# Kernel optimization log

Measured on AMD Instinct MI355X. Metric: run time of the kernel, lower is better.

Reference implementation:

```python
import jax, jax.numpy as jnp
import numpy as np


def setup_inputs() -> dict:
    key = jax.random.key(0)
    k1, k2, k3, k4, k5 = jax.random.split(key, 5)
    B, S, IN, OUT, R = 4, 2048, 4096, 4096, 16
    x = jax.random.normal(k1, (B, S, IN), dtype=jnp.float32)
    weight = jax.random.normal(k2, (OUT, IN), dtype=jnp.float32) * 0.02
    bias = jax.random.normal(k3, (OUT,), dtype=jnp.float32) * 0.02
    lora_A = jax.random.normal(k4, (R, IN), dtype=jnp.float32) * 0.02
    lora_B = jax.random.normal(k5, (OUT, R), dtype=jnp.float32) * 0.02
    return {"x": x, "weight": weight, "bias": bias, "lora_A": lora_A, "lora_B": lora_B}


def reference(x, weight, bias, lora_A, lora_B):
    # HiRA (Linear path): out = x @ (W * (1 + A^T B^T)^T)^T + bias
    # prod_AB[i, o] = sum_r A[r, i] * B[o, r]; adapted_weight[o, i] = W[o, i] * (prod_AB + 1)[i, o]
    prod_AB = jnp.einsum('ri,or->io', lora_A, lora_B) + 1.0       # [in, out]
    adapted_weight = weight * prod_AB.T                            # [out, in]
    # F.linear: x @ adapted_weight^T + bias
    return jnp.einsum('bsi,oi->bso', x, adapted_weight) + bias
```

## Files before the change

kernel.cpp:

```cpp
#include <hip/hip_runtime.h>
#include <hip/hip_bf16.h>
#include <stdint.h>

#define M_DIM 8192
#define N_DIM 4096
#define K_DIM 4096
#define R_DIM 16

typedef __bf16 bf16x8 __attribute__((ext_vector_type(8)));
typedef float f32x4 __attribute__((ext_vector_type(4)));
typedef unsigned short u16x8 __attribute__((ext_vector_type(8)));

#define AS1(p) ((const __attribute__((address_space(1))) void*)(p))
#define AS3(p) ((__attribute__((address_space(3))) void*)(p))

#define BAR() do { asm volatile("" ::: "memory"); __builtin_amdgcn_s_barrier(); asm volatile("" ::: "memory"); } while (0)
#define LGKM0() asm volatile("s_waitcnt lgkmcnt(0)" ::: "memory")
#define VMCNT6() asm volatile("s_waitcnt vmcnt(6)" ::: "memory")
#define VMCNT0() asm volatile("s_waitcnt vmcnt(0)" ::: "memory")

__device__ __forceinline__ unsigned short f2bf(float f) {
  unsigned u = __builtin_bit_cast(unsigned, f);
  u += 0x7FFFu + ((u >> 16) & 1u);
  return (unsigned short)(u >> 16);
}

#define CVT_BLOCKS 4096
__global__ void __launch_bounds__(256) prep_kernel(
    const float* __restrict__ x, const float* __restrict__ W,
    const float* __restrict__ lA, const float* __restrict__ lB,
    unsigned short* __restrict__ xb, unsigned short* __restrict__ awb) {
  __shared__ float Asub[16 * 512];
  __shared__ float Bsub[32 * 16];
  const int tid = threadIdx.x;

  if (blockIdx.x < 1024) {
    const int i0 = (blockIdx.x & 7) * 512;
    const int o0 = (blockIdx.x >> 3) * 32;
    for (int idx = tid; idx < 16 * 512; idx += 256) {
      int r = idx >> 9, i = idx & 511;
      Asub[idx] = lA[r * K_DIM + i0 + i];
    }
    for (int idx = tid; idx < 32 * 16; idx += 256) {
      int o = idx >> 4, r = idx & 15;
      Bsub[idx] = lB[(o0 + o) * R_DIM + r];
    }
    __syncthreads();
    for (int idx = tid; idx < 32 * 512; idx += 256) {
      int o = idx >> 9, i = idx & 511;
      float s = 1.0f;
#pragma unroll
      for (int r = 0; r < 16; ++r) s += Asub[r * 512 + i] * Bsub[o * 16 + r];
      size_t g = (size_t)(o0 + o) * K_DIM + i0 + i;
      awb[g] = f2bf(W[g] * s);
    }
  } else {
    const long total = (long)M_DIM * K_DIM;
    long i = ((long)(blockIdx.x - 1024) * 256 + tid) * 8;
    const long stride = (long)CVT_BLOCKS * 256 * 8;
    for (; i < total; i += stride) {
      const float4* p = (const float4*)(x + i);
      float4 f0 = p[0], f1 = p[1];
      u16x8 v;
      v[0] = f2bf(f0.x); v[1] = f2bf(f0.y); v[2] = f2bf(f0.z); v[3] = f2bf(f0.w);
      v[4] = f2bf(f1.x); v[5] = f2bf(f1.y); v[6] = f2bf(f1.z); v[7] = f2bf(f1.w);
      *(u16x8*)(xb + i) = v;
    }
  }
}

__global__ void __launch_bounds__(512, 2) gemm_kernel(
    const unsigned short* __restrict__ Ag,
    const unsigned short* __restrict__ Bg,
    const float* __restrict__ bias,
    float* __restrict__ out) {
  __shared__ __attribute__((aligned(16))) unsigned short LDS[2 * 32768];

  const int nwg = gridDim.x;
  const int q8 = nwg >> 3;
  const int wg = blockIdx.x;
  const int swz = (wg & 7) * q8 + (wg >> 3);
  const int tiles_n = N_DIM / 256;
  const int brow = (swz / tiles_n) * 256;
  const int bcol = (swz % tiles_n) * 256;

  const int tid = threadIdx.x;
  const int lane = tid & 63;
  const int w = tid >> 6;
  const int wr = w >> 2, wc = w & 3;
  const int fr = lane & 15;
  const int kq = (lane >> 4) << 3;

  const int rr = lane >> 2;
  const int cc = ((lane & 1) << 3) | ((((lane >> 1) ^ (lane >> 5)) & 1) << 4);
  const int c_sw = ((w & 1) << 5) | cc;
  const int rbase = ((w >> 1) << 4) + rr;

  const unsigned short* srcA[2][2];
#pragma unroll
  for (int h = 0; h < 2; ++h)
#pragma unroll
    for (int q = 0; q < 2; ++q)
      srcA[h][q] = Ag + (size_t)(brow + h * 128 + q * 64 + rbase) * K_DIM + c_sw;
  const long long bdelta = (long long)(Bg - Ag) + (long long)(bcol - brow) * K_DIM;

  auto stageA = [&](int buf, int h, int kt) {
#pragma unroll
    for (int q = 0; q < 2; ++q)
      __builtin_amdgcn_global_load_lds(AS1(srcA[h][q] + (size_t)kt * 64),
          AS3(&LDS[buf * 32768 + h * 8192 + q * 4096 + w * 512]), 16, 0, 0);
  };
  auto stageB = [&](int buf, int h, int kt) {
#pragma unroll
    for (int q = 0; q < 2; ++q)
      __builtin_amdgcn_global_load_lds(AS1(srcA[h][q] + bdelta + (size_t)kt * 64),
          AS3(&LDS[buf * 32768 + 16384 + h * 8192 + q * 4096 + w * 512]), 16, 0, 0);
  };

  const int rdsw = ((fr << 6) | (kq << 1)) ^ ((fr & 8) << 2);
  auto lda = [&](int buf, int m, int kk) -> bf16x8 {
    return *(const bf16x8*)((const char*)LDS +
        (buf * 65536 + wr * 16384 + (m * 2 + kk) * 1024 + rdsw));
  };
  auto ldb = [&](int buf, int n, int kk) -> bf16x8 {
    return *(const bf16x8*)((const char*)LDS +
        (buf * 65536 + 32768 + (wc >> 1) * 16384 +
         (((wc & 1) * 4 + n) * 2 + kk) * 1024 + rdsw));
  };

  f32x4 acc[8][4] = {};
  bf16x8 a[2][4], b[2][4];

  auto load_a_group = [&](int buf, int mg) {
#pragma unroll
    for (int kk = 0; kk < 2; ++kk)
#pragma unroll
      for (int mi = 0; mi < 4; ++mi)
        a[kk][mi] = lda(buf, mg + mi, kk);
  };
  auto load_b_pair = [&](int buf, int nb) {
#pragma unroll
    for (int kk = 0; kk < 2; ++kk)
#pragma unroll
      for (int ni = 0; ni < 2; ++ni)
        b[kk][nb + ni] = ldb(buf, nb + ni, kk);
  };
  auto mma_quad = [&](int mb, int nb) {
#pragma unroll
    for (int mi = 0; mi < 4; ++mi)
#pragma unroll
      for (int ni = 0; ni < 2; ++ni)
#pragma unroll
        for (int kk = 0; kk < 2; ++kk)
          acc[mb + mi][nb + ni] = __builtin_amdgcn_mfma_f32_16x16x32_bf16(
              a[kk][mi], b[kk][nb + ni], acc[mb + mi][nb + ni], 0, 0, 0);
  };

  stageB(0, 0, 0); stageB(0, 1, 0); stageA(0, 0, 0); stageA(0, 1, 0);
  stageB(1, 0, 1); stageB(1, 1, 1); stageA(1, 0, 1);
  VMCNT6();
  BAR();

#pragma unroll 1
  for (int i = 0; i < K_DIM / 128; ++i) {
    const bool more = (i < K_DIM / 128 - 1);
    const int t_cur1 = 2 * i + 1, t_nx0 = 2 * i + 2, t_nx1 = 2 * i + 3;

    load_a_group(0, 0); load_b_pair(0, 0);
    stageA(1, 1, t_cur1);
    BAR(); LGKM0();
    __builtin_amdgcn_s_setprio(1); mma_quad(0, 0); __builtin_amdgcn_s_setprio(0);
    BAR();
    load_b_pair(0, 2);
    BAR(); LGKM0();
    __builtin_amdgcn_s_setprio(1); mma_quad(0, 2); __builtin_amdgcn_s_setprio(0);
    BAR();
    load_a_group(0, 4);
    if (more) { stageB(0, 0, t_nx0); stageB(0, 1, t_nx0); }
    BAR(); LGKM0();
    __builtin_amdgcn_s_setprio(1); mma_quad(4, 2); __builtin_amdgcn_s_setprio(0);
    BAR();
    if (more) stageA(0, 0, t_nx0);
    BAR();
    __builtin_amdgcn_s_setprio(1); mma_quad(4, 0); __builtin_amdgcn_s_setprio(0);
    if (more) { VMCNT6(); } else { VMCNT0(); }
    BAR();

    load_a_group(1, 0); load_b_pair(1, 0);
    if (more) stageA(0, 1, t_nx0);
    BAR(); LGKM0();
    __builtin_amdgcn_s_setprio(1); mma_quad(0, 0); __builtin_amdgcn_s_setprio(0);
    BAR();
    load_b_pair(1, 2);
    BAR(); LGKM0();
    __builtin_amdgcn_s_setprio(1); mma_quad(0, 2); __builtin_amdgcn_s_setprio(0);
    BAR();
    load_a_group(1, 4);
    if (more) { stageB(1, 0, t_nx1); stageB(1, 1, t_nx1); }
    BAR(); LGKM0();
    __builtin_amdgcn_s_setprio(1); mma_quad(4, 2); __builtin_amdgcn_s_setprio(0);
    BAR();
    if (more) stageA(1, 0, t_nx1);
    BAR();
    __builtin_amdgcn_s_setprio(1); mma_quad(4, 0); __builtin_amdgcn_s_setprio(0);
    if (more) VMCNT6();
    BAR();
  }

  const int fq = (lane >> 4) * 4;
#pragma unroll
  for (int n = 0; n < 4; ++n) {
    const int col = bcol + wc * 64 + n * 16 + fr;
    const float bb = bias[col];
#pragma unroll
    for (int m = 0; m < 8; ++m) {
      const int row = brow + wr * 128 + m * 16 + fq;
      f32x4 v = acc[m][n];
#pragma unroll
      for (int j = 0; j < 4; ++j)
        out[(size_t)(row + j) * N_DIM + col] = v[j] + bb;
    }
  }
}

extern "C" void kernel_launch(void* const* d_in, const int* in_sizes, int n_in,
                              void* d_out, int out_size, void* d_ws, size_t ws_size,
                              hipStream_t stream) {
  const float* x    = (const float*)d_in[0];
  const float* W    = (const float*)d_in[1];
  const float* bias = (const float*)d_in[2];
  const float* lA   = (const float*)d_in[3];
  const float* lB   = (const float*)d_in[4];
  float* out = (float*)d_out;

  unsigned short* xb  = (unsigned short*)d_ws;
  unsigned short* awb = xb + (size_t)M_DIM * K_DIM;

  prep_kernel<<<1024 + CVT_BLOCKS, 256, 0, stream>>>(x, W, lA, lB, xb, awb);
  gemm_kernel<<<(M_DIM / 256) * (N_DIM / 256), 512, 0, stream>>>(xb, awb, bias, out);
}
```

Baseline: 302.6 us.

## Restructure GEMM main loop to prefetch next tile's LDS fragments during MFMAs

Rewrites the double-buffered GEMM K-loop so that LDS fragment reads for the next tile (A rows and both B halves) are issued while the MFMAs of the current tile run. B fragments are kept in separate lo/hi register sets so they can be refilled independently, and explicit lgkmcnt waits are dropped in favour of compiler-inserted ones. Global-to-LDS staging is reshuffled, the prologue now fills both buffers fully, and the vmcnt thresholds change to match. This aims to hide LDS latency and reduce barrier stalls, at the cost of more live registers and a tighter dependence on correct barrier and waitcnt ordering.

```diff
diff --git a/kernel.cpp b/kernel.cpp
--- a/kernel.cpp
+++ b/kernel.cpp
@@ -15,9 +15,9 @@
 #define AS3(p) ((__attribute__((address_space(3))) void*)(p))
 
 #define BAR() do { asm volatile("" ::: "memory"); __builtin_amdgcn_s_barrier(); asm volatile("" ::: "memory"); } while (0)
-#define LGKM0() asm volatile("s_waitcnt lgkmcnt(0)" ::: "memory")
-#define VMCNT6() asm volatile("s_waitcnt vmcnt(6)" ::: "memory")
+#define VMCNT2() asm volatile("s_waitcnt vmcnt(2)" ::: "memory")
 #define VMCNT0() asm volatile("s_waitcnt vmcnt(0)" ::: "memory")
+#define VMCNT8() asm volatile("s_waitcnt vmcnt(8)" ::: "memory")
 
 __device__ __forceinline__ unsigned short f2bf(float f) {
   unsigned u = __builtin_bit_cast(unsigned, f);
@@ -129,82 +129,71 @@
   };
 
   f32x4 acc[8][4] = {};
-  bf16x8 a[2][4], b[2][4];
-
-  auto load_a_group = [&](int buf, int mg) {
+  bf16x8 a[2][4];
+  bf16x8 blo[2][2], bhi[2][2];
+
+  auto read_a = [&](int buf, int mg) {
 #pragma unroll
     for (int kk = 0; kk < 2; ++kk)
 #pragma unroll
       for (int mi = 0; mi < 4; ++mi)
         a[kk][mi] = lda(buf, mg + mi, kk);
   };
-  auto load_b_pair = [&](int buf, int nb) {
+  auto read_blo = [&](int buf) {
 #pragma unroll
     for (int kk = 0; kk < 2; ++kk)
 #pragma unroll
       for (int ni = 0; ni < 2; ++ni)
-        b[kk][nb + ni] = ldb(buf, nb + ni, kk);
-  };
-  auto mma_quad = [&](int mb, int nb) {
+        blo[kk][ni] = ldb(buf, ni, kk);
+  };
+  auto read_bhi = [&](int buf) {
+#pragma unroll
+    for (int kk = 0; kk < 2; ++kk)
+#pragma unroll
+      for (int ni = 0; ni < 2; ++ni)
+        bhi[kk][ni] = ldb(buf, 2 + ni, kk);
+  };
+  auto mma_b = [&](bf16x8 (&bb)[2][2], int am, int an) {
 #pragma unroll
     for (int mi = 0; mi < 4; ++mi)
 #pragma unroll
       for (int ni = 0; ni < 2; ++ni)
 #pragma unroll
         for (int kk = 0; kk < 2; ++kk)
-          acc[mb + mi][nb + ni] = __builtin_amdgcn_mfma_f32_16x16x32_bf16(
-              a[kk][mi], b[kk][nb + ni], acc[mb + mi][nb + ni], 0, 0, 0);
+          acc[am + mi][an + ni] = __builtin_amdgcn_mfma_f32_16x16x32_bf16(
+              a[kk][mi], bb[kk][ni], acc[am + mi][an + ni], 0, 0, 0);
+  };
+
+  auto tile_body = [&](int t, int buf, bool g2, bool gr) {
+    const int nxbuf = buf ^ 1;
+    __builtin_amdgcn_s_setprio(1); mma_b(blo, 0, 0); __builtin_amdgcn_s_setprio(0);
+    BAR();
+    if (g2) stageB(buf, 0, t + 2);
+    __builtin_amdgcn_s_setprio(1); mma_b(bhi, 0, 2); __builtin_amdgcn_s_setprio(0);
+    read_a(buf, 4);
+    if (g2) { VMCNT2(); } else { VMCNT0(); }
+    BAR();
+    if (g2) { stageB(buf, 1, t + 2); stageA(buf, 0, t + 2); }
+    __builtin_amdgcn_s_setprio(1); mma_b(bhi, 4, 2); __builtin_amdgcn_s_setprio(0);
+    if (gr) read_bhi(nxbuf);
+    BAR();
+    if (g2) stageA(buf, 1, t + 2);
+    __builtin_amdgcn_s_setprio(1); mma_b(blo, 4, 0); __builtin_amdgcn_s_setprio(0);
+    if (gr) { read_a(nxbuf, 0); read_blo(nxbuf); }
+    BAR();
   };
 
   stageB(0, 0, 0); stageB(0, 1, 0); stageA(0, 0, 0); stageA(0, 1, 0);
-  stageB(1, 0, 1); stageB(1, 1, 1); stageA(1, 0, 1);
-  VMCNT6();
+  stageB(1, 0, 1); stageB(1, 1, 1); stageA(1, 0, 1); stageA(1, 1, 1);
+  VMCNT8();
   BAR();
+  read_bhi(0); read_a(0, 0); read_blo(0);
 
 #pragma unroll 1
-  for (int i = 0; i < K_DIM / 128; ++i) {
-    const bool more = (i < K_DIM / 128 - 1);
-    const int t_cur1 = 2 * i + 1, t_nx0 = 2 * i + 2, t_nx1 = 2 * i + 3;
-
-    load_a_group(0, 0); load_b_pair(0, 0);
-    stageA(1, 1, t_cur1);
-    BAR(); LGKM0();
-    __builtin_amdgcn_s_setprio(1); mma_quad(0, 0); __builtin_amdgcn_s_setprio(0);
-    BAR();
-    load_b_pair(0, 2);
-    BAR(); LGKM0();
-    __builtin_amdgcn_s_setprio(1); mma_quad(0, 2); __builtin_amdgcn_s_setprio(0);
-    BAR();
-    load_a_group(0, 4);
-    if (more) { stageB(0, 0, t_nx0); stageB(0, 1, t_nx0); }
-    BAR(); LGKM0();
-    __builtin_amdgcn_s_setprio(1); mma_quad(4, 2); __builtin_amdgcn_s_setprio(0);
-    BAR();
-    if (more) stageA(0, 0, t_nx0);
-    BAR();
-    __builtin_amdgcn_s_setprio(1); mma_quad(4, 0); __builtin_amdgcn_s_setprio(0);
-    if (more) { VMCNT6(); } else { VMCNT0(); }
-    BAR();
-
-    load_a_group(1, 0); load_b_pair(1, 0);
-    if (more) stageA(0, 1, t_nx0);
-    BAR(); LGKM0();
-    __builtin_amdgcn_s_setprio(1); mma_quad(0, 0); __builtin_amdgcn_s_setprio(0);
-    BAR();
-    load_b_pair(1, 2);
-    BAR(); LGKM0();
-    __builtin_amdgcn_s_setprio(1); mma_quad(0, 2); __builtin_amdgcn_s_setprio(0);
-    BAR();
-    load_a_group(1, 4);
-    if (more) { stageB(1, 0, t_nx1); stageB(1, 1, t_nx1); }
-    BAR(); LGKM0();
-    __builtin_amdgcn_s_setprio(1); mma_quad(4, 2); __builtin_amdgcn_s_setprio(0);
-    BAR();
-    if (more) stageA(1, 0, t_nx1);
-    BAR();
-    __builtin_amdgcn_s_setprio(1); mma_quad(4, 0); __builtin_amdgcn_s_setprio(0);
-    if (more) VMCNT6();
-    BAR();
+  for (int i = 0; i < 32; ++i) {
+    const bool more = (i < 31);
+    tile_body(2 * i,     0, more, true);
+    tile_body(2 * i + 1, 1, more, more);
   }
 
   const int fq = (lane >> 4) * 4;
```

New measurement: 294.1 us. -2.8%, faster.
